# Performance work log

Hardware: AMD Instinct MI355X
Metric: run time of the kernel (lower is better)

## Reference

```python
import jax, jax.numpy as jnp
import numpy as np
from jax import lax

STRIDES = (8, 16, 32)
FEAT_SIZES = ((80, 80), (40, 40), (20, 20))  # 640x640 input
NUM_CLASSES = 80
NMS_THR = 0.65
SCORE_THR = 0.01
NMS_PRE = 1000
MAX_PER_IMG = 100


def make_points():
    # MlvlPointGenerator.grid_priors with offset=0, with_stride=True.
    pts = []
    for (h, w), s in zip(FEAT_SIZES, STRIDES):
        y, x = jnp.meshgrid(jnp.arange(h, dtype=jnp.float32),
                            jnp.arange(w, dtype=jnp.float32), indexing='ij')
        pts.append(jnp.stack([x.ravel() * s, y.ravel() * s,
                              jnp.full(h * w, float(s)),
                              jnp.full(h * w, float(s))], axis=-1))
    return jnp.concatenate(pts, axis=0)  # [P, 4] = (px, py, sx, sy)


def decode_boxes(points, reg):
    # YOLOXBBoxDecoder: xy = reg[:2]*stride + point; wh = exp(reg[2:])*stride
    xys = reg[..., :2] * points[..., 2:] + points[..., :2]
    whs = jnp.exp(reg[..., 2:]) * points[..., 2:]
    half = whs * 0.5
    return jnp.concatenate([xys - half, xys + half], axis=-1)  # [..., 4] xyxy


def pairwise_iou(b):
    # b: [N, 4] xyxy
    area = (b[:, 2] - b[:, 0]) * (b[:, 3] - b[:, 1])
    lt = jnp.maximum(b[:, None, :2], b[None, :, :2])
    rb = jnp.minimum(b[:, None, 2:], b[None, :, 2:])
    wh = jnp.clip(rb - lt, 0.0)
    inter = wh[..., 0] * wh[..., 1]
    return inter / (area[:, None] + area[None, :] - inter + 1e-9)


def nms_image(cls_s, boxes, obj):
    # cls_s: [P, C] sigmoid scores, boxes: [P, 4], obj: [P] sigmoid objectness
    max_scores = jnp.max(cls_s, axis=-1)
    labels = jnp.argmax(cls_s, axis=-1)
    scores = max_scores * obj
    masked = jnp.where(scores >= SCORE_THR, scores, -1.0)
    top_scores, top_idx = lax.top_k(masked, NMS_PRE)  # sorted descending
    valid = top_scores >= SCORE_THR
    b = boxes[top_idx]            # [K, 4]
    lab = labels[top_idx]         # [K]
    # batched_nms: offset boxes per class so cross-class boxes never overlap
    off = lab.astype(b.dtype)[:, None] * (jnp.max(jnp.abs(b)) + 1.0)
    iou = pairwise_iou(b + off)   # [K, K]
    idx = jnp.arange(NMS_PRE)

    def body(i, keep):
        sup = (iou[i] > NMS_THR) & keep[i] & (idx > i)
        return keep & ~sup

    keep = lax.fori_loop(0, NMS_PRE, body, valid)
    # compact kept detections (score-sorted order preserved), pad to MAX_PER_IMG
    order = jnp.argsort(~keep, stable=True)[:MAX_PER_IMG]
    k = keep[order]
    out_b = jnp.where(k[:, None], b[order], 0.0)
    out_s = jnp.where(k, top_scores[order], 0.0)
    out_l = jnp.where(k, lab[order], -1)
    return out_b, out_s, out_l


def setup_inputs() -> dict:
    key = jax.random.key(0)
    ks = jax.random.split(key, 9)
    shapes = {
        'cls0': (32, NUM_CLASSES, 80, 80), 'cls1': (32, NUM_CLASSES, 40, 40),
        'cls2': (32, NUM_CLASSES, 20, 20),
        'reg0': (32, 4, 80, 80), 'reg1': (32, 4, 40, 40), 'reg2': (32, 4, 20, 20),
        'obj0': (32, 1, 80, 80), 'obj1': (32, 1, 40, 40), 'obj2': (32, 1, 20, 20),
    }
    return {n: jax.random.normal(k, s, dtype=jnp.float32)
            for (n, s), k in zip(shapes.items(), ks)}


def reference(cls0, cls1, cls2, reg0, reg1, reg2, obj0, obj1, obj2):
    def flat(xs, c):
        return jnp.concatenate(
            [jnp.transpose(x, (0, 2, 3, 1)).reshape(x.shape[0], -1, c) for x in xs],
            axis=1)
    cls = flat([cls0, cls1, cls2], NUM_CLASSES)   # [N, P, C]
    reg = flat([reg0, reg1, reg2], 4)             # [N, P, 4]
    obj = flat([obj0, obj1, obj2], 1)[..., 0]     # [N, P]
    points = make_points()                        # [P, 4]
    boxes = decode_boxes(points[None], reg)       # [N, P, 4]
    cls = jax.nn.sigmoid(cls)
    obj = jax.nn.sigmoid(obj)
    return jax.vmap(nms_image)(cls, boxes, obj)   # ([N,M,4],[N,M],[N,M] labels)
```

## Files before the change

kernel.cpp:

```cpp
#include <hip/hip_runtime.h>
#include <stdint.h>

#define N_IMG 32
#define P_TOT 8400
#define NCLS 80
#define NMS_PRE 1000
#define MAXOUT 100
#define SCORE_THRF 0.01f
#define NMS_THRF 0.65f
#define CAND_N 2048
#define NB 512
#define BINBASE 8192


__device__ __forceinline__ float sigmoidf_(float x) { return 1.0f / (1.0f + expf(-x)); }

__global__ __launch_bounds__(256) void k_score(
    const float* __restrict__ cls0, const float* __restrict__ cls1, const float* __restrict__ cls2,
    const float* __restrict__ obj0, const float* __restrict__ obj1, const float* __restrict__ obj2,
    uint64_t* __restrict__ keys)
{
    __shared__ uint64_t part[4][64];
    int lane = threadIdx.x & 63, wid = threadIdx.x >> 6;
    int a = blockIdx.x * 64 + lane;
    int n = a / P_TOT;
    int p = a - n * P_TOT;

    const float* cl; const float* ob; int HW, q;
    if (p < 6400)      { cl = cls0; ob = obj0; HW = 6400; q = p; }
    else if (p < 8000) { cl = cls1; ob = obj1; HW = 1600; q = p - 6400; }
    else               { cl = cls2; ob = obj2; HW = 400;  q = p - 8000; }

    const float* cbase = cl + (size_t)n * NCLS * HW + q;
    uint64_t m = 0;
    int c0 = wid * 20;
    #pragma unroll
    for (int i = 0; i < 20; ++i) {
        int c = c0 + i;
        float s = sigmoidf_(cbase[(size_t)c * HW]);
        uint64_t pk = ((uint64_t)__float_as_uint(s) << 8) | (uint32_t)(79 - c);
        m = m > pk ? m : pk;
    }
    part[wid][lane] = m;
    __syncthreads();

    if (wid == 0) {
        uint64_t m0 = part[0][lane], m1 = part[1][lane];
        uint64_t m2 = part[2][lane], m3 = part[3][lane];
        uint64_t ma = m0 > m1 ? m0 : m1, mb = m2 > m3 ? m2 : m3;
        uint64_t mm = ma > mb ? ma : mb;
        float best = __uint_as_float((uint32_t)(mm >> 8));
        int bc = 79 - (int)(mm & 0xFFu);

        float so = sigmoidf_(ob[(size_t)n * HW + q]);
        float sc = __fmul_rn(best, so);
        float masked = (sc >= SCORE_THRF) ? sc : -1.0f;
        uint32_t u = __float_as_uint(masked);
        uint32_t ord = (u & 0x80000000u) ? ~u : (u | 0x80000000u);
        uint32_t dk = ~ord;
        keys[a] = ((uint64_t)dk << 32) | (uint32_t)((p << 8) | bc);
    }
}

__global__ __launch_bounds__(1024) void k_select(
    const uint64_t* __restrict__ keys,
    uint64_t* __restrict__ skeys, int* __restrict__ nvalid)
{
    __shared__ uint32_t hist[NB];
    __shared__ uint32_t base[NB];
    __shared__ uint32_t fill[NB];
    __shared__ uint64_t grouped[CAND_N];
    __shared__ uint64_t cand[CAND_N];
    __shared__ int      s_misc[2];

    int n = blockIdx.x, tid = threadIdx.x;

    if (tid < NB) { hist[tid] = 0; fill[tid] = 0; }
    for (int t = tid; t < CAND_N; t += 1024) cand[t] = ~0ull;
    __syncthreads();

    #pragma unroll
    for (int it = 0; it < 9; ++it) {
        int t = tid + it * 1024;
        if (t < P_TOT) {
            uint64_t k = keys[(size_t)n * P_TOT + t];
            uint32_t dk = (uint32_t)(k >> 32);
            if (!(dk & 0x80000000u)) atomicAdd(&hist[(dk >> 17) - BINBASE], 1u);
        }
    }
    __syncthreads();

    if (tid < 64) {
        uint32_t c[8]; uint32_t s = 0;
        #pragma unroll
        for (int i = 0; i < 8; ++i) { c[i] = hist[tid * 8 + i]; s += c[i]; }
        uint32_t inc = s;
        #pragma unroll
        for (int o = 1; o < 64; o <<= 1) {
            uint32_t v = __shfl_up(inc, o);
            if (tid >= o) inc += v;
        }
        uint32_t excl = inc - s;
        uint32_t b = excl;
        #pragma unroll
        for (int i = 0; i < 8; ++i) { base[tid * 8 + i] = b; b += c[i]; }
        uint32_t total = __shfl(inc, 63);
        uint32_t target = total < (uint32_t)NMS_PRE ? total : (uint32_t)NMS_PRE;
        uint32_t cum = excl; int found = 0x7fffffff;
        #pragma unroll
        for (int i = 0; i < 8; ++i) {
            cum += c[i];
            if (found == 0x7fffffff && cum >= target && target > 0) found = tid * 8 + i;
        }
        #pragma unroll
        for (int o = 32; o > 0; o >>= 1) { int f = __shfl_xor(found, o); found = f < found ? f : found; }
        if (tid == 0) { s_misc[0] = (total > 0) ? found : -1; s_misc[1] = (int)target; }
    }
    __syncthreads();
    int Bcut = s_misc[0];

    #pragma unroll
    for (int it = 0; it < 9; ++it) {
        int t = tid + it * 1024;
        if (t < P_TOT) {
            uint64_t k = keys[(size_t)n * P_TOT + t];
            uint32_t dk = (uint32_t)(k >> 32);
            if (!(dk & 0x80000000u)) {
                int bin = (int)((dk >> 17) - BINBASE);
                if (bin <= Bcut) {
                    uint32_t pos = base[bin] + atomicAdd(&fill[bin], 1u);
                    if (pos < CAND_N) grouped[pos] = k;
                }
            }
        }
    }
    __syncthreads();

    int ccnt = 0;
    if (Bcut >= 0) {
        uint32_t cc = base[Bcut] + hist[Bcut];
        ccnt = cc < (uint32_t)CAND_N ? (int)cc : CAND_N;
    }
    for (int s = tid; s < ccnt; s += 1024) {
        uint64_t k = grouped[s];
        uint32_t dk = (uint32_t)(k >> 32);
        int bin = (int)((dk >> 17) - BINBASE);
        uint32_t b0 = base[bin];
        uint32_t e0 = b0 + hist[bin]; if (e0 > (uint32_t)CAND_N) e0 = CAND_N;
        uint32_t r = b0;
        for (uint32_t t = b0; t < e0; ++t) r += (grouped[t] < k) ? 1u : 0u;
        if (r < (uint32_t)CAND_N) cand[r] = k;
    }
    __syncthreads();

    if (tid < NMS_PRE) skeys[n * NMS_PRE + tid] = cand[tid];
    if (tid == 0) nvalid[n] = s_misc[1];
}

__global__ __launch_bounds__(256) void k_nms(
    const uint64_t* __restrict__ skeys, const int* __restrict__ nvalid,
    const float* __restrict__ reg0, const float* __restrict__ reg1, const float* __restrict__ reg2,
    float* __restrict__ out)
{
    __shared__ float4 s_obx[NMS_PRE];
    __shared__ float4 s_raw[NMS_PRE];
    __shared__ float2 s_sl[NMS_PRE];
    __shared__ float  s_oar[NMS_PRE];
    __shared__ float  fsh[4];
    __shared__ int    kidx[MAXOUT];

    int n = blockIdx.x, tid = threadIdx.x;
    int lane = tid & 63, wv = tid >> 6;
    int V = nvalid[n];

    float4 bx4[4]; float scm4[4], lab4[4];
    float m = 0.f;
    #pragma unroll
    for (int it = 0; it < 4; ++it) {
        int t = tid + it * 256;
        float4 bx = make_float4(0.f, 0.f, 0.f, 0.f);
        float scm = -1.0f, labf = 0.f;
        if (t < NMS_PRE) {
            uint64_t key = skeys[n * NMS_PRE + t];
            uint32_t dk = (uint32_t)(key >> 32);
            if (!(dk & 0x80000000u)) {
                uint32_t low = (uint32_t)key;
                int lab = (int)(low & 0xFFu);
                int p   = (int)(low >> 8);
                uint32_t ord = ~dk;
                scm = __uint_as_float(ord ^ 0x80000000u);

                const float* rg; int HW, q, W; float s;
                if (p < 6400)      { rg = reg0; HW = 6400; q = p;        W = 80; s = 8.f; }
                else if (p < 8000) { rg = reg1; HW = 1600; q = p - 6400; W = 40; s = 16.f; }
                else               { rg = reg2; HW = 400;  q = p - 8000; W = 20; s = 32.f; }

                float px = (float)(q % W) * s;
                float py = (float)(q / W) * s;
                const float* rb = rg + (size_t)n * 4 * HW + q;
                float dx = rb[0], dy = rb[HW], dw = rb[2 * HW], dh = rb[3 * HW];
                float cx = __fadd_rn(__fmul_rn(dx, s), px);
                float cy = __fadd_rn(__fmul_rn(dy, s), py);
                float hw = __fmul_rn(__fmul_rn(expf(dw), s), 0.5f);
                float hh = __fmul_rn(__fmul_rn(expf(dh), s), 0.5f);
                bx.x = __fsub_rn(cx, hw); bx.y = __fsub_rn(cy, hh);
                bx.z = __fadd_rn(cx, hw); bx.w = __fadd_rn(cy, hh);
                labf = (float)lab;
                m = fmaxf(m, fmaxf(fmaxf(fabsf(bx.x), fabsf(bx.y)), fmaxf(fabsf(bx.z), fabsf(bx.w))));
            }
            s_raw[t] = bx;
            s_sl[t]  = make_float2(scm, labf);
        }
        bx4[it] = bx; scm4[it] = scm; lab4[it] = labf;
    }

    #pragma unroll
    for (int o = 32; o > 0; o >>= 1) m = fmaxf(m, __shfl_xor(m, o));
    if (lane == 0) fsh[wv] = m;
    __syncthreads();
    float gmax = fmaxf(fmaxf(fsh[0], fsh[1]), fmaxf(fsh[2], fsh[3]));

    #pragma unroll
    for (int it = 0; it < 4; ++it) {
        int t = tid + it * 256;
        if (t < NMS_PRE) {
            float off = __fmul_rn(lab4[it], __fadd_rn(gmax, 1.0f));
            float x1 = __fadd_rn(bx4[it].x, off), y1 = __fadd_rn(bx4[it].y, off);
            float x2 = __fadd_rn(bx4[it].z, off), y2 = __fadd_rn(bx4[it].w, off);
            s_obx[t] = make_float4(x1, y1, x2, y2);
            s_oar[t] = __fmul_rn(__fsub_rn(x2, x1), __fsub_rn(y2, y1));
        }
    }
    __syncthreads();
    if (tid >= 64) return;

    int count = 0;
    float k1x1 = 0.f, k1y1 = 0.f, k1x2 = 0.f, k1y2 = 0.f, k1a = 0.f;
    float k2x1 = 0.f, k2y1 = 0.f, k2x2 = 0.f, k2y2 = 0.f, k2a = 0.f;

    float4 nb = s_obx[0]; float na = s_oar[0];
    for (int i = 0; i < V && count < MAXOUT; ++i) {
        float4 cb = nb; float ca = na;
        int ip = (i + 1 < V) ? i + 1 : i;
        nb = s_obx[ip]; na = s_oar[ip];

        bool sup = false;
        int c1 = count < 64 ? count : 64;
        if (lane < c1) {
            float ltx = fmaxf(k1x1, cb.x), lty = fmaxf(k1y1, cb.y);
            float rbx = fminf(k1x2, cb.z), rby = fminf(k1y2, cb.w);
            float w = fmaxf(__fsub_rn(rbx, ltx), 0.f);
            float h = fmaxf(__fsub_rn(rby, lty), 0.f);
            float inter = __fmul_rn(w, h);
            float denom = __fadd_rn(__fsub_rn(__fadd_rn(k1a, ca), inter), 1e-9f);
            sup = (inter / denom > NMS_THRF);
        }
        if (count > 64 && lane < count - 64) {
            float ltx = fmaxf(k2x1, cb.x), lty = fmaxf(k2y1, cb.y);
            float rbx = fminf(k2x2, cb.z), rby = fminf(k2y2, cb.w);
            float w = fmaxf(__fsub_rn(rbx, ltx), 0.f);
            float h = fmaxf(__fsub_rn(rby, lty), 0.f);
            float inter = __fmul_rn(w, h);
            float denom = __fadd_rn(__fsub_rn(__fadd_rn(k2a, ca), inter), 1e-9f);
            sup = sup || (inter / denom > NMS_THRF);
        }
        if (__ballot(sup) == 0ull) {
            if (lane == count)      { k1x1 = cb.x; k1y1 = cb.y; k1x2 = cb.z; k1y2 = cb.w; k1a = ca; }
            if (lane + 64 == count) { k2x1 = cb.x; k2y1 = cb.y; k2x2 = cb.z; k2y2 = cb.w; k2a = ca; }
            if (lane == 0) kidx[count] = i;
            ++count;
        }
    }

    float* ob = out;
    float* os = out + N_IMG * MAXOUT * 4;
    float* ol = os + N_IMG * MAXOUT;
    for (int mi = lane; mi < MAXOUT; mi += 64) {
        int o4 = (n * MAXOUT + mi) * 4;
        if (mi < count) {
            int i = kidx[mi];
            float4 b  = s_raw[i];
            float2 sl = s_sl[i];
            ob[o4 + 0] = b.x; ob[o4 + 1] = b.y; ob[o4 + 2] = b.z; ob[o4 + 3] = b.w;
            os[n * MAXOUT + mi] = sl.x;
            ol[n * MAXOUT + mi] = sl.y;
        } else {
            ob[o4 + 0] = 0.f; ob[o4 + 1] = 0.f; ob[o4 + 2] = 0.f; ob[o4 + 3] = 0.f;
            os[n * MAXOUT + mi] = 0.f;
            ol[n * MAXOUT + mi] = -1.f;
        }
    }
}

extern "C" void kernel_launch(void* const* d_in, const int* in_sizes, int n_in,
                              void* d_out, int out_size, void* d_ws, size_t ws_size,
                              hipStream_t stream)
{
    const float* cls0 = (const float*)d_in[0];
    const float* cls1 = (const float*)d_in[1];
    const float* cls2 = (const float*)d_in[2];
    const float* reg0 = (const float*)d_in[3];
    const float* reg1 = (const float*)d_in[4];
    const float* reg2 = (const float*)d_in[5];
    const float* obj0 = (const float*)d_in[6];
    const float* obj1 = (const float*)d_in[7];
    const float* obj2 = (const float*)d_in[8];

    uint64_t* keys  = (uint64_t*)d_ws;
    uint64_t* skeys = (uint64_t*)((char*)d_ws + (4u << 20));
    int*     nvalid = (int*)((char*)d_ws + (4u << 20) + (512u << 10));
    float* out = (float*)d_out;

    k_score<<<(N_IMG * P_TOT) / 64, 256, 0, stream>>>(
        cls0, cls1, cls2, obj0, obj1, obj2, keys);
    k_select<<<N_IMG, 1024, 0, stream>>>(keys, skeys, nvalid);
    k_nms<<<N_IMG, 256, 0, stream>>>(skeys, nvalid, reg0, reg1, reg2, out);
}
```

Baseline: 76.68 us.

## Rework score kernel: two anchors per thread, raw-logit max prefilter, lazy sigmoid

```diff
diff --git a/kernel.cpp b/kernel.cpp
--- a/kernel.cpp
+++ b/kernel.cpp
@@ -11,6 +11,9 @@
 #define CAND_N 2048
 #define NB 512
 #define BINBASE 8192
+#define TIE_EPS 0.05f
+#define NBATCH 8
+#define BSZ 10
 
 
 __device__ __forceinline__ float sigmoidf_(float x) { return 1.0f / (1.0f + expf(-x)); }
@@ -20,11 +23,10 @@
     const float* __restrict__ obj0, const float* __restrict__ obj1, const float* __restrict__ obj2,
     uint64_t* __restrict__ keys)
 {
-    __shared__ uint64_t part[4][64];
-    int lane = threadIdx.x & 63, wid = threadIdx.x >> 6;
-    int a = blockIdx.x * 64 + lane;
-    int n = a / P_TOT;
-    int p = a - n * P_TOT;
+    int t = blockIdx.x * 256 + threadIdx.x;
+    int a0 = t * 2;
+    int n = a0 / P_TOT;
+    int p = a0 - n * P_TOT;
 
     const float* cl; const float* ob; int HW, q;
     if (p < 6400)      { cl = cls0; ob = obj0; HW = 6400; q = p; }
@@ -32,34 +34,66 @@
     else               { cl = cls2; ob = obj2; HW = 400;  q = p - 8000; }
 
     const float* cbase = cl + (size_t)n * NCLS * HW + q;
-    uint64_t m = 0;
-    int c0 = wid * 20;
-    #pragma unroll
-    for (int i = 0; i < 20; ++i) {
-        int c = c0 + i;
-        float s = sigmoidf_(cbase[(size_t)c * HW]);
-        uint64_t pk = ((uint64_t)__float_as_uint(s) << 8) | (uint32_t)(79 - c);
-        m = m > pk ? m : pk;
-    }
-    part[wid][lane] = m;
-    __syncthreads();
-
-    if (wid == 0) {
-        uint64_t m0 = part[0][lane], m1 = part[1][lane];
-        uint64_t m2 = part[2][lane], m3 = part[3][lane];
-        uint64_t ma = m0 > m1 ? m0 : m1, mb = m2 > m3 ? m2 : m3;
-        uint64_t mm = ma > mb ? ma : mb;
-        float best = __uint_as_float((uint32_t)(mm >> 8));
-        int bc = 79 - (int)(mm & 0xFFu);
-
-        float so = sigmoidf_(ob[(size_t)n * HW + q]);
-        float sc = __fmul_rn(best, so);
+
+    float bmx[NBATCH], bmy[NBATCH];
+    float gx = -3.4e38f, gy = -3.4e38f;
+    #pragma unroll
+    for (int b = 0; b < NBATCH; ++b) {
+        float2 v[BSZ];
+        #pragma unroll
+        for (int i = 0; i < BSZ; ++i)
+            v[i] = *reinterpret_cast<const float2*>(cbase + (size_t)(b * BSZ + i) * HW);
+        __builtin_amdgcn_sched_group_barrier(0x20, BSZ, 0);
+        float ax0 = fmaxf(v[0].x, v[1].x), ax1 = fmaxf(v[2].x, v[3].x);
+        float ax2 = fmaxf(v[4].x, v[5].x), ax3 = fmaxf(v[6].x, v[7].x);
+        float ax4 = fmaxf(v[8].x, v[9].x);
+        float ay0 = fmaxf(v[0].y, v[1].y), ay1 = fmaxf(v[2].y, v[3].y);
+        float ay2 = fmaxf(v[4].y, v[5].y), ay3 = fmaxf(v[6].y, v[7].y);
+        float ay4 = fmaxf(v[8].y, v[9].y);
+        float bx = fmaxf(fmaxf(fmaxf(ax0, ax1), fmaxf(ax2, ax3)), ax4);
+        float by = fmaxf(fmaxf(fmaxf(ay0, ay1), fmaxf(ay2, ay3)), ay4);
+        bmx[b] = bx; bmy[b] = by;
+        gx = fmaxf(gx, bx); gy = fmaxf(gy, by);
+    }
+
+    float tx = gx - TIE_EPS, ty = gy - TIE_EPS;
+    uint64_t m0 = 0, m1 = 0;
+    #pragma unroll
+    for (int b = 0; b < NBATCH; ++b) {
+        bool need = (bmx[b] >= tx) || (bmy[b] >= ty);
+        if (__any(need)) {
+            #pragma unroll
+            for (int i = 0; i < BSZ; ++i) {
+                float2 v = *reinterpret_cast<const float2*>(cbase + (size_t)(b * BSZ + i) * HW);
+                uint32_t ct = (uint32_t)(79 - (b * BSZ + i));
+                if (v.x >= tx) { uint64_t pk = ((uint64_t)__float_as_uint(sigmoidf_(v.x)) << 8) | ct; m0 = m0 > pk ? m0 : pk; }
+                if (v.y >= ty) { uint64_t pk = ((uint64_t)__float_as_uint(sigmoidf_(v.y)) << 8) | ct; m1 = m1 > pk ? m1 : pk; }
+            }
+        }
+    }
+
+    float2 ov = *reinterpret_cast<const float2*>(ob + (size_t)n * HW + q);
+    float sox = sigmoidf_(ov.x), soy = sigmoidf_(ov.y);
+    uint64_t kk[2];
+    {
+        float best = __uint_as_float((uint32_t)(m0 >> 8));
+        int bc = 79 - (int)(m0 & 0xFFu);
+        float sc = __fmul_rn(best, sox);
         float masked = (sc >= SCORE_THRF) ? sc : -1.0f;
         uint32_t u = __float_as_uint(masked);
         uint32_t ord = (u & 0x80000000u) ? ~u : (u | 0x80000000u);
-        uint32_t dk = ~ord;
-        keys[a] = ((uint64_t)dk << 32) | (uint32_t)((p << 8) | bc);
-    }
+        kk[0] = ((uint64_t)(~ord) << 32) | (uint32_t)((p << 8) | bc);
+    }
+    {
+        float best = __uint_as_float((uint32_t)(m1 >> 8));
+        int bc = 79 - (int)(m1 & 0xFFu);
+        float sc = __fmul_rn(best, soy);
+        float masked = (sc >= SCORE_THRF) ? sc : -1.0f;
+        uint32_t u = __float_as_uint(masked);
+        uint32_t ord = (u & 0x80000000u) ? ~u : (u | 0x80000000u);
+        kk[1] = ((uint64_t)(~ord) << 32) | (uint32_t)(((p + 1) << 8) | bc);
+    }
+    *reinterpret_cast<ulonglong2*>(keys + a0) = make_ulonglong2(kk[0], kk[1]);
 }
 
 __global__ __launch_bounds__(1024) void k_select(
@@ -173,7 +207,7 @@
     int lane = tid & 63, wv = tid >> 6;
     int V = nvalid[n];
 
-    float4 bx4[4]; float scm4[4], lab4[4];
+    float4 bx4[4]; float lab4[4];
     float m = 0.f;
     #pragma unroll
     for (int it = 0; it < 4; ++it) {
@@ -211,7 +245,7 @@
             s_raw[t] = bx;
             s_sl[t]  = make_float2(scm, labf);
         }
-        bx4[it] = bx; scm4[it] = scm; lab4[it] = labf;
+        bx4[it] = bx; lab4[it] = labf;
     }
 
     #pragma unroll
@@ -311,7 +345,7 @@
     int*     nvalid = (int*)((char*)d_ws + (4u << 20) + (512u << 10));
     float* out = (float*)d_out;
 
-    k_score<<<(N_IMG * P_TOT) / 64, 256, 0, stream>>>(
+    k_score<<<525, 256, 0, stream>>>(
         cls0, cls1, cls2, obj0, obj1, obj2, keys);
     k_select<<<N_IMG, 1024, 0, stream>>>(keys, skeys, nvalid);
     k_nms<<<N_IMG, 256, 0, stream>>>(skeys, nvalid, reg0, reg1, reg2, out);
```

Result: slower. 120.7 us (+57.4%).

## Split class-max into top-2 logit partial pass and merge with sigmoid-tie fallback

Applied to the files above, without the earlier changes.

```diff
diff --git a/kernel.cpp b/kernel.cpp
--- a/kernel.cpp
+++ b/kernel.cpp
@@ -11,55 +11,119 @@
 #define CAND_N 2048
 #define NB 512
 #define BINBASE 8192
+#define TIE_EPS 0.05f
+#define CHUNKS 5
+#define TILES 9
 
 
 __device__ __forceinline__ float sigmoidf_(float x) { return 1.0f / (1.0f + expf(-x)); }
-
-__global__ __launch_bounds__(256) void k_score(
+__device__ __forceinline__ uint32_t ordmap_(uint32_t u) {
+    return (u & 0x80000000u) ? ~u : (u | 0x80000000u);
+}
+__device__ __forceinline__ float unord_(uint32_t o) {
+    return __uint_as_float((o & 0x80000000u) ? (o ^ 0x80000000u) : ~o);
+}
+__device__ __forceinline__ void merge2_(uint64_t& a1, uint64_t& a2, uint64_t b1, uint64_t b2) {
+    uint64_t lo = a1 < b1 ? a1 : b1;
+    a1 = a1 > b1 ? a1 : b1;
+    uint64_t m2 = a2 > b2 ? a2 : b2;
+    a2 = lo > m2 ? lo : m2;
+}
+
+__global__ __launch_bounds__(1024) void k_pmax(
+    const float* __restrict__ cls0, const float* __restrict__ cls1, const float* __restrict__ cls2,
+    ulonglong2* __restrict__ part)
+{
+    __shared__ float stage[16][256];
+    int bid = blockIdx.x;
+    int n = bid / (TILES * CHUNKS);
+    int r = bid - n * (TILES * CHUNKS);
+    int tile = r / CHUNKS, ch = r - tile * CHUNKS;
+    int wid = threadIdx.x >> 6, lane = threadIdx.x & 63;
+    int cls = ch * 16 + wid;
+
+    for (int seg = 0; seg < 4; ++seg) {
+        int abase = tile * 1024 + seg * 256;
+        int p0 = abase + lane * 4;
+        if (p0 < P_TOT) {
+            const float* cl; int HW, q0;
+            if (p0 < 6400)      { cl = cls0; HW = 6400; q0 = p0; }
+            else if (p0 < 8000) { cl = cls1; HW = 1600; q0 = p0 - 6400; }
+            else                { cl = cls2; HW = 400;  q0 = p0 - 8000; }
+            float4 v = *reinterpret_cast<const float4*>(
+                cl + (size_t)n * NCLS * HW + (size_t)cls * HW + q0);
+            *reinterpret_cast<float4*>(&stage[wid][lane * 4]) = v;
+        }
+        __syncthreads();
+        if (threadIdx.x < 256) {
+            int a = threadIdx.x;
+            int p = abase + a;
+            if (p < P_TOT) {
+                uint64_t t1 = 0, t2 = 0;
+                #pragma unroll
+                for (int k = 0; k < 16; ++k) {
+                    uint32_t ord = ordmap_(__float_as_uint(stage[k][a]));
+                    uint64_t pk = ((uint64_t)ord << 8) | (uint32_t)(79 - (ch * 16 + k));
+                    uint64_t lo = t1 < pk ? t1 : pk;
+                    t1 = t1 > pk ? t1 : pk;
+                    t2 = t2 > lo ? t2 : lo;
+                }
+                part[(size_t)ch * (N_IMG * P_TOT) + (size_t)n * P_TOT + p] =
+                    make_ulonglong2(t1, t2);
+            }
+        }
+        __syncthreads();
+    }
+}
+
+__global__ __launch_bounds__(256) void k_merge(
+    const ulonglong2* __restrict__ part,
     const float* __restrict__ cls0, const float* __restrict__ cls1, const float* __restrict__ cls2,
     const float* __restrict__ obj0, const float* __restrict__ obj1, const float* __restrict__ obj2,
     uint64_t* __restrict__ keys)
 {
-    __shared__ uint64_t part[4][64];
-    int lane = threadIdx.x & 63, wid = threadIdx.x >> 6;
-    int a = blockIdx.x * 64 + lane;
-    int n = a / P_TOT;
-    int p = a - n * P_TOT;
+    int a = blockIdx.x * 256 + threadIdx.x;
+    if (a >= N_IMG * P_TOT) return;
+    int n = a / P_TOT, p = a - n * P_TOT;
+
+    uint64_t t1 = 0, t2 = 0;
+    #pragma unroll
+    for (int c = 0; c < CHUNKS; ++c) {
+        ulonglong2 v = part[(size_t)c * (N_IMG * P_TOT) + a];
+        merge2_(t1, t2, v.x, v.y);
+    }
+    float l1 = unord_((uint32_t)(t1 >> 8));
+    float l2 = unord_((uint32_t)(t2 >> 8));
 
     const float* cl; const float* ob; int HW, q;
     if (p < 6400)      { cl = cls0; ob = obj0; HW = 6400; q = p; }
     else if (p < 8000) { cl = cls1; ob = obj1; HW = 1600; q = p - 6400; }
     else               { cl = cls2; ob = obj2; HW = 400;  q = p - 8000; }
 
-    const float* cbase = cl + (size_t)n * NCLS * HW + q;
-    uint64_t m = 0;
-    int c0 = wid * 20;
-    #pragma unroll
-    for (int i = 0; i < 20; ++i) {
-        int c = c0 + i;
-        float s = sigmoidf_(cbase[(size_t)c * HW]);
-        uint64_t pk = ((uint64_t)__float_as_uint(s) << 8) | (uint32_t)(79 - c);
-        m = m > pk ? m : pk;
-    }
-    part[wid][lane] = m;
-    __syncthreads();
-
-    if (wid == 0) {
-        uint64_t m0 = part[0][lane], m1 = part[1][lane];
-        uint64_t m2 = part[2][lane], m3 = part[3][lane];
-        uint64_t ma = m0 > m1 ? m0 : m1, mb = m2 > m3 ? m2 : m3;
-        uint64_t mm = ma > mb ? ma : mb;
-        float best = __uint_as_float((uint32_t)(mm >> 8));
-        int bc = 79 - (int)(mm & 0xFFu);
-
-        float so = sigmoidf_(ob[(size_t)n * HW + q]);
-        float sc = __fmul_rn(best, so);
-        float masked = (sc >= SCORE_THRF) ? sc : -1.0f;
-        uint32_t u = __float_as_uint(masked);
-        uint32_t ord = (u & 0x80000000u) ? ~u : (u | 0x80000000u);
-        uint32_t dk = ~ord;
-        keys[a] = ((uint64_t)dk << 32) | (uint32_t)((p << 8) | bc);
-    }
+    float best; int bc;
+    if (l2 < l1 - TIE_EPS) {
+        best = sigmoidf_(l1);
+        bc = 79 - (int)(t1 & 0xFFu);
+    } else {
+        const float* cbase = cl + (size_t)n * NCLS * HW + q;
+        uint64_t m = 0;
+        #pragma unroll 8
+        for (int c = 0; c < NCLS; ++c) {
+            float s = sigmoidf_(cbase[(size_t)c * HW]);
+            uint64_t pk = ((uint64_t)__float_as_uint(s) << 8) | (uint32_t)(79 - c);
+            m = m > pk ? m : pk;
+        }
+        best = __uint_as_float((uint32_t)(m >> 8));
+        bc = 79 - (int)(m & 0xFFu);
+    }
+
+    float so = sigmoidf_(ob[(size_t)n * HW + q]);
+    float sc = __fmul_rn(best, so);
+    float masked = (sc >= SCORE_THRF) ? sc : -1.0f;
+    uint32_t u = __float_as_uint(masked);
+    uint32_t ord = (u & 0x80000000u) ? ~u : (u | 0x80000000u);
+    uint32_t dk = ~ord;
+    keys[a] = ((uint64_t)dk << 32) | (uint32_t)((p << 8) | bc);
 }
 
 __global__ __launch_bounds__(1024) void k_select(
@@ -173,7 +237,7 @@
     int lane = tid & 63, wv = tid >> 6;
     int V = nvalid[n];
 
-    float4 bx4[4]; float scm4[4], lab4[4];
+    float4 bx4[4]; float lab4[4];
     float m = 0.f;
     #pragma unroll
     for (int it = 0; it < 4; ++it) {
@@ -211,7 +275,7 @@
             s_raw[t] = bx;
             s_sl[t]  = make_float2(scm, labf);
         }
-        bx4[it] = bx; scm4[it] = scm; lab4[it] = labf;
+        bx4[it] = bx; lab4[it] = labf;
     }
 
     #pragma unroll
@@ -306,13 +370,15 @@
     const float* obj1 = (const float*)d_in[7];
     const float* obj2 = (const float*)d_in[8];
 
-    uint64_t* keys  = (uint64_t*)d_ws;
-    uint64_t* skeys = (uint64_t*)((char*)d_ws + (4u << 20));
-    int*     nvalid = (int*)((char*)d_ws + (4u << 20) + (512u << 10));
+    uint64_t*   keys   = (uint64_t*)d_ws;
+    uint64_t*   skeys  = (uint64_t*)((char*)d_ws + (4u << 20));
+    int*        nvalid = (int*)((char*)d_ws + (4u << 20) + (512u << 10));
+    ulonglong2* part   = (ulonglong2*)((char*)d_ws + (8u << 20));
     float* out = (float*)d_out;
 
-    k_score<<<(N_IMG * P_TOT) / 64, 256, 0, stream>>>(
-        cls0, cls1, cls2, obj0, obj1, obj2, keys);
+    k_pmax<<<N_IMG * TILES * CHUNKS, 1024, 0, stream>>>(cls0, cls1, cls2, part);
+    k_merge<<<(N_IMG * P_TOT + 255) / 256, 256, 0, stream>>>(
+        part, cls0, cls1, cls2, obj0, obj1, obj2, keys);
     k_select<<<N_IMG, 1024, 0, stream>>>(keys, skeys, nvalid);
     k_nms<<<N_IMG, 256, 0, stream>>>(skeys, nvalid, reg0, reg1, reg2, out);
 }
```

After: 105.1 us. +37.0%, slower.
